# Kernel tuning notes

Measured on AMD Instinct MI355X. Metric: run time of the kernel, lower is better.

## Reference

```python
import math
import jax, jax.numpy as jnp
import numpy as np


def setup_inputs() -> dict:
    key = jax.random.key(0)
    ks = jax.random.split(key, 6)
    B, L, d_model = 8, 4096, 512
    s = 1.0 / math.sqrt(d_model)
    inp = {
        "x": jax.random.normal(ks[0], (B, L, d_model), dtype=jnp.float32),
        "Wq": jax.random.normal(ks[1], (d_model, d_model), dtype=jnp.float32) * s,
        "bq": jnp.zeros((d_model,), jnp.float32),
        "Wk": jax.random.normal(ks[2], (d_model, d_model), dtype=jnp.float32) * s,
        "bk": jnp.zeros((d_model,), jnp.float32),
        "Wv": jax.random.normal(ks[3], (d_model, d_model), dtype=jnp.float32) * s,
        "bv": jnp.zeros((d_model,), jnp.float32),
        "Wo": jax.random.normal(ks[4], (d_model, d_model), dtype=jnp.float32) * s,
        "bo": jnp.zeros((d_model,), jnp.float32),
    }
    return inp


N_HEADS = 8
FACTOR = 1


def reference(x, Wq, bq, Wk, bk, Wv, bv, Wo, bo):
    B, L, d_model = x.shape
    H = N_HEADS
    D = d_model // H
    # projections (torch Linear: x @ W.T + b), reshape to (B,H,L,D)
    def proj(W, b):
        y = jnp.einsum("bld,ed->ble", x, W) + b
        return y.reshape(B, L, H, D).transpose(0, 2, 1, 3)
    q = proj(Wq, bq)
    k = proj(Wk, bk)
    v = proj(Wv, bv)
    # FFT autocorrelation along time axis (axis=2)
    q_f = jnp.fft.rfft(q, axis=2)
    k_f = jnp.fft.rfft(k, axis=2)
    corr = jnp.fft.irfft(q_f * jnp.conj(k_f), n=L, axis=2)  # (B,H,L,D)
    k_top = max(1, int(FACTOR * math.log(L + 1)))
    k_top = min(k_top, L)
    corr_mean = corr.mean(axis=-1)  # (B,H,L)
    top_vals, top_idx = jax.lax.top_k(corr_mean, k_top)  # (B,H,k)
    weights = jax.nn.softmax(top_vals, axis=-1)  # (B,H,k)
    t = jnp.arange(L).reshape(1, 1, 1, L)
    idx = (t + top_idx[..., None]) % L  # (B,H,k,L)
    # gather rolled V per selected lag: (B,H,k,L,D)
    v_exp = jnp.broadcast_to(v[:, :, None], (B, H, k_top, L, D))
    gathered = jnp.take_along_axis(v_exp, idx[..., None], axis=3)
    out = jnp.einsum("bhkld,bhk->bhld", gathered, weights)
    out = out.transpose(0, 2, 1, 3).reshape(B, L, d_model)
    # dropout=0.0 (eval): identity
    return jnp.einsum("bld,ed->ble", out, Wo) + bo
```

## Files before the change

### kernel.cpp

```cpp
#include <hip/hip_runtime.h>
#include <cstdint>
#include <cstddef>

#define AS1 __attribute__((address_space(1)))
#define AS3 __attribute__((address_space(3)))

using half8  = __attribute__((ext_vector_type(8))) _Float16;
using half4v = __attribute__((ext_vector_type(4))) _Float16;
using half2v = __attribute__((ext_vector_type(2))) _Float16;
using f32x4  = __attribute__((ext_vector_type(4))) float;

__global__ void prep_all_kernel(const float* __restrict__ x,
                                const float* __restrict__ Wq, const float* __restrict__ Wk,
                                const float* __restrict__ Wv, const float* __restrict__ Wo,
                                const float* __restrict__ bq, const float* __restrict__ bk,
                                const float* __restrict__ bv,
                                _Float16* __restrict__ xh, _Float16* __restrict__ Bt,
                                _Float16* __restrict__ WoH,
                                float2* __restrict__ tw, float* __restrict__ bias) {
    const int bid = blockIdx.x;
    const int tid = threadIdx.x;
    if (bid < 16384) {
        int i = (bid * 256 + tid) * 4;
        float4 v = *(const float4*)(x + i);
        half4v h;
        h[0] = (_Float16)v.x; h[1] = (_Float16)v.y;
        h[2] = (_Float16)v.z; h[3] = (_Float16)v.w;
        *(half4v*)(xh + i) = h;
    } else if (bid < 19456) {
        int i = (bid - 16384) * 256 + tid;
        int e = i >> 9, k = i & 511;
        int proj = e >> 9, er = e & 511;
        const float* W = (proj == 0) ? Wq : ((proj == 1) ? Wk : Wv);
        Bt[i] = (_Float16)W[er * 512 + k];
    } else if (bid < 20480) {
        int i = (bid - 19456) * 256 + tid;
        WoH[i] = (_Float16)Wo[i];
    } else if (bid < 20496) {
        int p = (bid - 20480) * 256 + tid;
        double th = -2.0 * 3.14159265358979323846 * (double)p / 4096.0;
        tw[p] = make_float2((float)cos(th), (float)sin(th));
    } else {
        int i = (bid - 20496) * 256 + tid;
        bias[i] = (i < 512) ? bq[i] : ((i < 1024) ? bk[i - 512] : bv[i - 1024]);
    }
}

template <int MODE>
__global__ __launch_bounds__(512, 2) void gemm_f16_kernel(
    const _Float16* __restrict__ A, const _Float16* __restrict__ Bt,
    const float* __restrict__ bias,
    _Float16* __restrict__ qT, _Float16* __restrict__ kT,
    _Float16* __restrict__ vout, float* __restrict__ Cout)
{
    constexpr int NBLK   = (MODE == 0) ? 6 : 2;
    constexpr int PERXCD = (MODE == 0) ? 96 : 32;
    __shared__ _Float16 smem[65536];

    const int gi = (blockIdx.x & 7) * PERXCD + (blockIdx.x >> 3);
    const int mb = gi / NBLK;
    const int nb = gi - mb * NBLK;
    const int m0 = mb * 256, n0 = nb * 256;
    const int tid = threadIdx.x;
    const int wave = tid >> 6, lane = tid & 63;
    const int lane15 = lane & 15, quad = lane >> 4;
    const int wmr = (wave >> 2) * 128;
    const int wnr = (wave & 3) * 64;

    const int r0 = tid >> 2;
    const int c0 = (tid & 3) ^ ((tid >> 3) & 3);
    const char* gA = (const char*)A  + ((size_t)(m0 + r0)) * 1024 + c0 * 16;
    const char* gB = (const char*)Bt + ((size_t)(n0 + r0)) * 1024 + c0 * 16;
    const int sbw = wave * 1024;
    const int coloff = (quad ^ ((lane15 >> 1) & 3)) << 4;

    f32x4 acc[8][4];
#pragma unroll
    for (int mi = 0; mi < 8; mi++)
#pragma unroll
        for (int ni = 0; ni < 4; ni++)
#pragma unroll
            for (int r = 0; r < 4; r++) acc[mi][ni][r] = 0.f;

    auto STAGE = [&](int slot, int tensor, int kk, int kt) {
        const char* g = (tensor == 0 ? gA : gB) + kt * 128 + kk * 64;
        char* base = (char*)smem + slot * 65536 + tensor * 32768 + kk * 16384 + sbw;
        __builtin_amdgcn_global_load_lds((const AS1 void*)g, (AS3 void*)base, 16, 0, 0);
        __builtin_amdgcn_global_load_lds((const AS1 void*)(g + 131072), (AS3 void*)(base + 8192), 16, 0, 0);
    };

    half8 af[4], bf[4];
    auto LOADA = [&](int slot, int kk, int mh) {
        const char* ba = (const char*)smem + slot * 65536 + kk * 16384;
#pragma unroll
        for (int j = 0; j < 4; j++)
            af[j] = *(const half8*)(ba + (wmr + (mh * 4 + j) * 16 + lane15) * 64 + coloff);
    };
    auto LOADB = [&](int slot, int kk) {
        const char* bb = (const char*)smem + slot * 65536 + 32768 + kk * 16384;
#pragma unroll
        for (int j = 0; j < 4; j++)
            bf[j] = *(const half8*)(bb + (wnr + j * 16 + lane15) * 64 + coloff);
    };
    auto MMA = [&](int mh) {
        __builtin_amdgcn_s_setprio(1);
#pragma unroll
        for (int j = 0; j < 4; j++)
#pragma unroll
            for (int ni = 0; ni < 4; ni++)
                acc[mh * 4 + j][ni] =
                    __builtin_amdgcn_mfma_f32_16x16x32_f16(af[j], bf[ni], acc[mh * 4 + j][ni], 0, 0, 0);
        __builtin_amdgcn_s_setprio(0);
    };
#define BAR() do { __builtin_amdgcn_s_barrier(); asm volatile("" ::: "memory"); } while (0)
#define VMW(n) asm volatile("s_waitcnt vmcnt(" #n ")" ::: "memory")

    STAGE(0, 0, 0, 0); STAGE(0, 1, 0, 0);
    STAGE(0, 0, 1, 0); STAGE(0, 1, 1, 0);
    STAGE(1, 0, 0, 1); STAGE(1, 1, 0, 1);
    VMW(8);
    BAR();

    for (int t = 0; t < 6; ++t) {
        const int slot = t & 1, nslot = slot ^ 1;
        LOADA(slot, 0, 0); LOADB(slot, 0);
        STAGE(nslot, 0, 1, t + 1);
        BAR(); MMA(0); BAR();
        LOADA(slot, 0, 1);
        STAGE(nslot, 1, 1, t + 1);
        BAR(); MMA(1);
        VMW(8);
        BAR();
        LOADA(slot, 1, 0); LOADB(slot, 1);
        STAGE(slot, 0, 0, t + 2);
        BAR(); MMA(0); BAR();
        LOADA(slot, 1, 1);
        STAGE(slot, 1, 0, t + 2);
        BAR(); MMA(1);
        VMW(8);
        BAR();
    }
    LOADA(0, 0, 0); LOADB(0, 0); STAGE(1, 0, 1, 7); BAR(); MMA(0); BAR();
    LOADA(0, 0, 1);              STAGE(1, 1, 1, 7); BAR(); MMA(1);
    VMW(8); BAR();
    LOADA(0, 1, 0); LOADB(0, 1); BAR(); MMA(0); BAR();
    LOADA(0, 1, 1);              BAR(); MMA(1);
    VMW(4);
    BAR();
    LOADA(1, 0, 0); LOADB(1, 0); BAR(); MMA(0); BAR();
    LOADA(1, 0, 1);              BAR(); MMA(1);
    VMW(0);
    BAR();
    LOADA(1, 1, 0); LOADB(1, 1); BAR(); MMA(0); BAR();
    LOADA(1, 1, 1);              BAR(); MMA(1);
#undef BAR
#undef VMW

    if (MODE == 1) {
#pragma unroll
        for (int mi = 0; mi < 8; mi++)
#pragma unroll
            for (int ni = 0; ni < 4; ni++) {
                const int n = n0 + wnr + ni * 16 + lane15;
                const float bb = bias[n];
#pragma unroll
                for (int r = 0; r < 4; r++) {
                    const int m = m0 + wmr + mi * 16 + quad * 4 + r;
                    Cout[(size_t)m * 512 + n] = acc[mi][ni][r] + bb;
                }
            }
        return;
    }
    const int proj = n0 >> 9;
    if (proj == 2) {
#pragma unroll
        for (int mi = 0; mi < 8; mi++)
#pragma unroll
            for (int ni = 0; ni < 4; ni++) {
                const int n = n0 + wnr + ni * 16 + lane15;
                const int er = n - 1024, h = er >> 6, d = er & 63;
                const float bb = bias[n];
#pragma unroll
                for (int r = 0; r < 4; r++) {
                    const int m = m0 + wmr + mi * 16 + quad * 4 + r;
                    const int b = m >> 12, l = m & 4095;
                    vout[((size_t)((b * 8 + h) * 4096 + l)) * 64 + d] = (_Float16)(acc[mi][ni][r] + bb);
                }
            }
        return;
    }
    _Float16* dst = (proj == 0) ? qT : kT;
    const int b = m0 >> 12;
    const int lbase = (m0 & 4095) + wmr + quad * 4;
#pragma unroll
    for (int mi = 0; mi < 8; mi++)
#pragma unroll
        for (int ni = 0; ni < 4; ni++) {
            const int e = n0 + wnr + ni * 16 + lane15;
            const int er = e & 511, h = er >> 6, d = er & 63;
            const float bb = bias[e];
            half4v o;
            o[0] = (_Float16)(acc[mi][ni][0] + bb);
            o[1] = (_Float16)(acc[mi][ni][1] + bb);
            o[2] = (_Float16)(acc[mi][ni][2] + bb);
            o[3] = (_Float16)(acc[mi][ni][3] + bb);
            *(half4v*)(dst + ((size_t)((b * 8 + h) * 64 + d)) * 4096 + lbase + mi * 16) = o;
        }
}

__device__ __forceinline__ float2 cmul(float2 a, float2 b) {
    return make_float2(a.x * b.x - a.y * b.y, a.x * b.y + a.y * b.x);
}
__device__ __forceinline__ float2 cmulc(float2 a, float cr, float ci) {
    return make_float2(a.x * cr - a.y * ci, a.x * ci + a.y * cr);
}
__device__ __forceinline__ int swz(int i) { return i ^ ((i >> 4) & 15); }

__device__ __forceinline__ void dft16(float2 x[16]) {
    constexpr float wc[10] = {1.f, 0.92387953f, 0.70710678f, 0.38268343f, 0.f,
                              0.f, -0.70710678f, 0.f, 0.f, -0.92387953f};
    constexpr float wsn[10] = {0.f, -0.38268343f, -0.70710678f, -0.92387953f, -1.f,
                               0.f, -0.70710678f, 0.f, 0.f, 0.38268343f};
    float2 t[16];
#pragma unroll
    for (int u = 0; u < 4; u++) {
        const float2 a = x[u], b = x[u + 4], c = x[u + 8], d = x[u + 12];
        const float2 Ea = make_float2(a.x + c.x, a.y + c.y);
        const float2 Oa = make_float2(a.x - c.x, a.y - c.y);
        const float2 Eb = make_float2(b.x + d.x, b.y + d.y);
        const float2 Ob = make_float2(b.x - d.x, b.y - d.y);
        const float2 y0 = make_float2(Ea.x + Eb.x, Ea.y + Eb.y);
        const float2 y1 = make_float2(Oa.x + Ob.y, Oa.y - Ob.x);
        const float2 y2 = make_float2(Ea.x - Eb.x, Ea.y - Eb.y);
        const float2 y3 = make_float2(Oa.x - Ob.y, Oa.y + Ob.x);
        t[4 * u + 0] = y0;
        t[4 * u + 1] = cmulc(y1, wc[u * 1], wsn[u * 1]);
        t[4 * u + 2] = cmulc(y2, wc[u * 2], wsn[u * 2]);
        t[4 * u + 3] = cmulc(y3, wc[u * 3], wsn[u * 3]);
    }
#pragma unroll
    for (int v = 0; v < 4; v++) {
        const float2 a = t[v], b = t[v + 4], c = t[v + 8], d = t[v + 12];
        const float2 Ea = make_float2(a.x + c.x, a.y + c.y);
        const float2 Oa = make_float2(a.x - c.x, a.y - c.y);
        const float2 Eb = make_float2(b.x + d.x, b.y + d.y);
        const float2 Ob = make_float2(b.x - d.x, b.y - d.y);
        x[v]      = make_float2(Ea.x + Eb.x, Ea.y + Eb.y);
        x[v + 4]  = make_float2(Oa.x + Ob.y, Oa.y - Ob.x);
        x[v + 8]  = make_float2(Ea.x - Eb.x, Ea.y - Eb.y);
        x[v + 12] = make_float2(Oa.x - Ob.y, Oa.y + Ob.x);
    }
}

__device__ __forceinline__ void fft4096_r16(float2* buf, const float2* __restrict__ tw,
                                            int tid, float2 (&x)[16]) {
    __syncthreads();
#pragma unroll
    for (int j = 0; j < 16; j++) x[j] = buf[swz(tid + 256 * j)];
    __syncthreads();
    dft16(x);
    buf[swz(16 * tid)] = x[0];
#pragma unroll
    for (int m = 1; m < 16; m++) buf[swz(16 * tid + m)] = cmul(x[m], tw[tid * m]);
    __syncthreads();
#pragma unroll
    for (int j = 0; j < 16; j++) x[j] = buf[swz(tid + 256 * j)];
    __syncthreads();
    dft16(x);
    {
        const int q = tid & 15, p = tid >> 4;
        const int base = q + 256 * p;
        buf[swz(base)] = x[0];
#pragma unroll
        for (int m = 1; m < 16; m++)
            buf[swz(base + 16 * m)] = cmul(x[m], tw[(p * m) << 4]);
    }
    __syncthreads();
#pragma unroll
    for (int j = 0; j < 16; j++) x[j] = buf[swz(tid + 256 * j)];
    __syncthreads();
    dft16(x);
#pragma unroll
    for (int m = 0; m < 16; m++) buf[swz(tid + 256 * m)] = x[m];
    __syncthreads();
}

__global__ __launch_bounds__(256) void fft_partial_kernel(
    const _Float16* __restrict__ qT, const _Float16* __restrict__ kT,
    const float2* __restrict__ tw, float2* __restrict__ spec)
{
    __shared__ float2 buf[4096];
    const int tid = threadIdx.x;
    const int bh = blockIdx.x >> 4, chunk = blockIdx.x & 15;
    float sx[16], sy[16];
#pragma unroll
    for (int i = 0; i < 16; i++) { sx[i] = 0.f; sy[i] = 0.f; }
    const _Float16* qb = qT + (size_t)bh * 64 * 4096;
    const _Float16* kb = kT + (size_t)bh * 64 * 4096;
    float2 x[16];
    for (int dd = 0; dd < 4; dd++) {
        const int d = chunk * 4 + dd;
#pragma unroll
        for (int i = 0; i < 2; i++) {
            const int t0 = 2048 * i + tid * 8;
            const half8 fq = *(const half8*)(qb + d * 4096 + t0);
            const half8 fk = *(const half8*)(kb + d * 4096 + t0);
#pragma unroll
            for (int j = 0; j < 8; j++)
                buf[swz(t0 + j)] = make_float2((float)fq[j], (float)fk[j]);
        }
        fft4096_r16(buf, tw, tid, x);
#pragma unroll
        for (int i = 0; i < 16; i++) {
            const int f = tid + 256 * i;
            const float2 Zf = x[i];
            const float2 Zm = buf[swz((4096 - f) & 4095)];
            const float Qr  = 0.5f * (Zf.x + Zm.x);
            const float Qi  = 0.5f * (Zf.y - Zm.y);
            const float cKr = 0.5f * (Zf.y + Zm.y);
            const float cKi = 0.5f * (Zf.x - Zm.x);
            sx[i] += Qr * cKr - Qi * cKi;
            sy[i] += Qr * cKi + Qi * cKr;
        }
        __syncthreads();
    }
    float2* out = spec + (size_t)blockIdx.x * 4096;
#pragma unroll
    for (int i = 0; i < 16; i++) out[tid + 256 * i] = make_float2(sx[i], sy[i]);
}

__global__ __launch_bounds__(256) void sum_spec_kernel(
    const float4* __restrict__ spec4, float4* __restrict__ ssum4)
{
    const int bh = blockIdx.x >> 3;
    const int i4 = (blockIdx.x & 7) * 256 + threadIdx.x;
    const float4* base = spec4 + (size_t)bh * 16 * 2048 + i4;
    float4 s = make_float4(0.f, 0.f, 0.f, 0.f);
#pragma unroll
    for (int c = 0; c < 16; c++) {
        const float4 v = base[(size_t)c * 2048];
        s.x += v.x; s.y += v.y; s.z += v.z; s.w += v.w;
    }
    s.y = -s.y; s.w = -s.w;
    ssum4[(size_t)bh * 2048 + i4] = s;
}

__global__ __launch_bounds__(256) void reduce_topk_kernel(
    const float2* __restrict__ ssum, const float2* __restrict__ tw,
    int* __restrict__ top_idx, float* __restrict__ top_w)
{
    __shared__ float2 buf[4096];
    __shared__ float wv[4];
    __shared__ int wi[4];
    const int tid = threadIdx.x;
    const int bh = blockIdx.x;
#pragma unroll
    for (int i = 0; i < 16; i++) {
        const int f = tid + 256 * i;
        buf[swz(f)] = ssum[(size_t)bh * 4096 + f];
    }
    float2 x[16];
    fft4096_r16(buf, tw, tid, x);
    float vals[8]; int idxs[8];
    for (int k = 0; k < 8; k++) {
        float best = -3.0e38f; int bi = 0;
#pragma unroll
        for (int i = 0; i < 16; i++) {
            const int f = tid + 256 * i;
            const float c = buf[swz(f)].x;
            if (c > best) { best = c; bi = f; }
        }
#pragma unroll
        for (int off = 32; off > 0; off >>= 1) {
            const float ov = __shfl_down(best, off);
            const int oi = __shfl_down(bi, off);
            if (ov > best || (ov == best && oi < bi)) { best = ov; bi = oi; }
        }
        if ((tid & 63) == 0) { wv[tid >> 6] = best; wi[tid >> 6] = bi; }
        __syncthreads();
        if (tid == 0) {
            best = wv[0]; bi = wi[0];
            for (int w = 1; w < 4; w++) {
                if (wv[w] > best || (wv[w] == best && wi[w] < bi)) { best = wv[w]; bi = wi[w]; }
            }
            vals[k] = best; idxs[k] = bi;
            buf[swz(bi)].x = -3.4e38f;
        }
        __syncthreads();
    }
    if (tid == 0) {
        const float scale = 1.f / (4096.f * 64.f);
        float e[8], s = 0.f;
        const float mx = vals[0] * scale;
        for (int k = 0; k < 8; k++) { e[k] = __expf(vals[k] * scale - mx); s += e[k]; }
        for (int k = 0; k < 8; k++) {
            top_w[bh * 8 + k] = e[k] / s;
            top_idx[bh * 8 + k] = idxs[k];
        }
    }
}

__global__ __launch_bounds__(256) void gather_kernel(
    const half8* __restrict__ v8, const int* __restrict__ top_idx,
    const float* __restrict__ top_w, half8* __restrict__ out8)
{
    const int gi = (blockIdx.x & 7) * 1024 + (blockIdx.x >> 3);
    const int bh = gi >> 7;
    const int lgrp = gi & 127;
    const int b = bh >> 3, h = bh & 7;
    const int tid = threadIdx.x;
    const int l = lgrp * 32 + (tid >> 3);
    const int d8 = tid & 7;
    int idx[8]; float w[8];
#pragma unroll
    for (int k = 0; k < 8; k++) { idx[k] = top_idx[bh * 8 + k]; w[k] = top_w[bh * 8 + k]; }
    const half8* vb = v8 + (size_t)bh * 4096 * 8;
    float a[8];
#pragma unroll
    for (int j = 0; j < 8; j++) a[j] = 0.f;
#pragma unroll
    for (int k = 0; k < 8; k++) {
        const int ls = (l + idx[k]) & 4095;
        const half8 pv = vb[(size_t)ls * 8 + d8];
#pragma unroll
        for (int j = 0; j < 8; j++) a[j] += w[k] * (float)pv[j];
    }
    half8 o;
#pragma unroll
    for (int j = 0; j < 8; j++) o[j] = (_Float16)a[j];
    out8[((size_t)(b * 4096 + l)) * 64 + h * 8 + d8] = o;
}

extern "C" void kernel_launch(void* const* d_in, const int* in_sizes, int n_in,
                              void* d_out, int out_size, void* d_ws, size_t ws_size,
                              hipStream_t stream) {
    (void)in_sizes; (void)n_in; (void)out_size; (void)ws_size;
    const float* x  = (const float*)d_in[0];
    const float* Wq = (const float*)d_in[1];
    const float* bq = (const float*)d_in[2];
    const float* Wk = (const float*)d_in[3];
    const float* bk = (const float*)d_in[4];
    const float* Wv = (const float*)d_in[5];
    const float* bv = (const float*)d_in[6];
    const float* Wo = (const float*)d_in[7];
    const float* bo = (const float*)d_in[8];
    float* out = (float*)d_out;

    char* ws = (char*)d_ws;
    size_t off = 0;
    auto alloc = [&](size_t bytes) -> void* {
        void* p = ws + off; off += (bytes + 255) & ~(size_t)255; return p;
    };
    _Float16* xh   = (_Float16*)alloc(33554432);
    _Float16* qT   = (_Float16*)alloc(33554432);
    _Float16* kT   = (_Float16*)alloc(33554432);
    _Float16* vbuf = (_Float16*)alloc(33554432);
    float2* spec   = (float2*)alloc(33554432);
    float2* ssum   = (float2*)alloc(2097152);
    _Float16* BtH  = (_Float16*)alloc(1572864);
    _Float16* WoH  = (_Float16*)alloc(524288);
    float* biasQKV = (float*)alloc(6144);
    float2* tw     = (float2*)alloc(32768);
    int*   top_idx = (int*)alloc(2048);
    float* top_w   = (float*)alloc(2048);
    _Float16* out_pre = xh;

    prep_all_kernel<<<20502, 256, 0, stream>>>(x, Wq, Wk, Wv, Wo, bq, bk, bv,
                                               xh, BtH, WoH, tw, biasQKV);
    gemm_f16_kernel<0><<<768, 512, 0, stream>>>(xh, BtH, biasQKV, qT, kT, vbuf, nullptr);
    fft_partial_kernel<<<1024, 256, 0, stream>>>(qT, kT, tw, spec);
    sum_spec_kernel<<<512, 256, 0, stream>>>((const float4*)spec, (float4*)ssum);
    reduce_topk_kernel<<<64, 256, 0, stream>>>(ssum, tw, top_idx, top_w);
    gather_kernel<<<8192, 256, 0, stream>>>((const half8*)vbuf, top_idx, top_w,
                                            (half8*)out_pre);
    gemm_f16_kernel<1><<<256, 512, 0, stream>>>(out_pre, WoH, bo, nullptr, nullptr, nullptr, out);
}
```

Baseline: 310.7 us.

## Compute per-wave local top-8 in registers, merge once; linearize gather block order

The top-k selection no longer runs eight block-wide rounds with two barriers each. Each wavefront now holds its 16 values per thread in registers, picks its own top-8 candidates using only wave shuffles, and writes them to shared memory; a single thread then merges the 32 candidates after one barrier. The gather kernel also drops its interleaved block-index remap and uses a linear mapping, which changes how blocks are placed and what cache locality they get. The merge is serial on one thread, and the change in gather block order could help or hurt L2 reuse.

```diff
diff --git a/kernel.cpp b/kernel.cpp
--- a/kernel.cpp
+++ b/kernel.cpp
@@ -350,8 +350,8 @@
     int* __restrict__ top_idx, float* __restrict__ top_w)
 {
     __shared__ float2 buf[4096];
-    __shared__ float wv[4];
-    __shared__ int wi[4];
+    __shared__ float cval[32];
+    __shared__ int cidx[32];
     const int tid = threadIdx.x;
     const int bh = blockIdx.x;
 #pragma unroll
@@ -361,14 +361,16 @@
     }
     float2 x[16];
     fft4096_r16(buf, tw, tid, x);
-    float vals[8]; int idxs[8];
+    const int wid = tid >> 6;
+    float c[16];
+#pragma unroll
+    for (int i = 0; i < 16; i++) c[i] = buf[swz(tid + 256 * i)].x;
     for (int k = 0; k < 8; k++) {
         float best = -3.0e38f; int bi = 0;
 #pragma unroll
         for (int i = 0; i < 16; i++) {
             const int f = tid + 256 * i;
-            const float c = buf[swz(f)].x;
-            if (c > best) { best = c; bi = f; }
+            if (c[i] > best) { best = c[i]; bi = f; }
         }
 #pragma unroll
         for (int off = 32; off > 0; off >>= 1) {
@@ -376,19 +378,25 @@
             const int oi = __shfl_down(bi, off);
             if (ov > best || (ov == best && oi < bi)) { best = ov; bi = oi; }
         }
-        if ((tid & 63) == 0) { wv[tid >> 6] = best; wi[tid >> 6] = bi; }
-        __syncthreads();
-        if (tid == 0) {
-            best = wv[0]; bi = wi[0];
-            for (int w = 1; w < 4; w++) {
-                if (wv[w] > best || (wv[w] == best && wi[w] < bi)) { best = wv[w]; bi = wi[w]; }
+        best = __shfl(best, 0); bi = __shfl(bi, 0);
+        if ((tid & 63) == 0) { cval[wid * 8 + k] = best; cidx[wid * 8 + k] = bi; }
+        const int ii = bi >> 8;
+#pragma unroll
+        for (int i = 0; i < 16; i++)
+            if (i == ii && tid == (bi & 255)) c[i] = -3.4e38f;
+    }
+    __syncthreads();
+    if (tid == 0) {
+        float vals[8]; int idxs[8];
+        for (int k = 0; k < 8; k++) {
+            float best = -3.0e38f; int bi = 0; int bc = 0;
+            for (int cc = 0; cc < 32; cc++) {
+                const float v = cval[cc]; const int ix = cidx[cc];
+                if (v > best || (v == best && ix < bi)) { best = v; bi = ix; bc = cc; }
             }
+            cval[bc] = -3.4e38f;
             vals[k] = best; idxs[k] = bi;
-            buf[swz(bi)].x = -3.4e38f;
-        }
-        __syncthreads();
-    }
-    if (tid == 0) {
+        }
         const float scale = 1.f / (4096.f * 64.f);
         float e[8], s = 0.f;
         const float mx = vals[0] * scale;
@@ -404,9 +412,9 @@
     const half8* __restrict__ v8, const int* __restrict__ top_idx,
     const float* __restrict__ top_w, half8* __restrict__ out8)
 {
-    const int gi = (blockIdx.x & 7) * 1024 + (blockIdx.x >> 3);
-    const int bh = gi >> 7;
-    const int lgrp = gi & 127;
+    const int seq = blockIdx.x;
+    const int bh = seq >> 7;
+    const int lgrp = seq & 127;
     const int b = bh >> 3, h = bh & 7;
     const int tid = threadIdx.x;
     const int l = lgrp * 32 + (tid >> 3);
```

Result: slower. 338.0 us (+8.8%).
